# Kernel tuning notes

Hardware: AMD Instinct MI355X
Metric: run time of the kernel (lower is better)

## Reference

```python
import jax, jax.numpy as jnp
import numpy as np

B, S, H, U = 32, 2048, 1024, 1024


def setup_inputs() -> dict:
    key = jax.random.key(0)
    ks = jax.random.split(key, 8)
    sH = 1.0 / np.sqrt(H)
    sU = 1.0 / np.sqrt(U)
    return {
        "encoder_output": jax.random.normal(ks[0], (B, S, H), dtype=jnp.float32),
        "last_layer_h_n": jax.random.normal(ks[1], (B, H), dtype=jnp.float32),
        # torch Linear stores weight [out,in]; we store transposed [in,out] for x @ W
        "W1_w": jax.random.uniform(ks[2], (H, U), jnp.float32, -sH, sH),
        "W1_b": jax.random.uniform(ks[3], (U,), jnp.float32, -sH, sH),
        "W2_w": jax.random.uniform(ks[4], (H, U), jnp.float32, -sH, sH),
        "W2_b": jax.random.uniform(ks[5], (U,), jnp.float32, -sH, sH),
        "V_w": jax.random.uniform(ks[6], (U, 1), jnp.float32, -sU, sU),
        "V_b": jax.random.uniform(ks[7], (1,), jnp.float32, -sU, sU),
    }


def reference(encoder_output, last_layer_h_n, W1_w, W1_b, W2_w, W2_b, V_w, V_b):
    # proj_enc: [B,S,U]; proj_h: [B,1,U] (unsqueeze(1) broadcast)
    proj_enc = jnp.einsum("bsh,hu->bsu", encoder_output, W1_w) + W1_b
    proj_h = (last_layer_h_n @ W2_w + W2_b)[:, None, :]
    # score: [B,S,1]
    score = jnp.tanh(proj_enc + proj_h) @ V_w + V_b
    # softmax over the sequence axis (dim 1)
    attention_weights = jax.nn.softmax(score, axis=1)
    # NOTE: in the original module context_vector is always None (dead branch),
    # so the faithful output is attention_weights alone.
    return attention_weights
```

## Files before the change

kernel.cpp:

```cpp
#include <hip/hip_runtime.h>
#include <hip/hip_bf16.h>


typedef __bf16 bf16x8 __attribute__((ext_vector_type(8)));
typedef float  f32x4  __attribute__((ext_vector_type(4)));

#define HDIM 1024
#define UDIM 1024
#define SDIM 2048
#define MROWS 65536
#define BM 128
#define BN 128
#define BK 32
#define LDK 40

__device__ inline unsigned short f2bf(float x) {
    return __builtin_bit_cast(unsigned short, (__bf16)x);
}

__global__ void w1t_kernel(const float* __restrict__ W1, unsigned short* __restrict__ W1T) {
    __shared__ float tile[32][33];
    int bx = blockIdx.x;
    int by = blockIdx.y;
    int tx = threadIdx.x, ty = threadIdx.y;
#pragma unroll
    for (int r = 0; r < 4; ++r) {
        int h = by * 32 + ty + r * 8;
        int u = bx * 32 + tx;
        tile[ty + r * 8][tx] = W1[h * UDIM + u];
    }
    __syncthreads();
#pragma unroll
    for (int r = 0; r < 4; ++r) {
        int u = bx * 32 + ty + r * 8;
        int h = by * 32 + tx;
        W1T[u * HDIM + h] = f2bf(tile[tx][ty + r * 8]);
    }
}

__global__ void php_kernel(const float* __restrict__ hn, const float* __restrict__ W2,
                           float* __restrict__ php) {
    int u = (blockIdx.x & 3) * 256 + threadIdx.x;
    int b = blockIdx.y;
    int hc = blockIdx.z;
    int h0 = hc * 128;
    float acc = 0.f;
#pragma unroll 8
    for (int h = h0; h < h0 + 128; ++h)
        acc = fmaf(hn[b * HDIM + h], W2[h * UDIM + u], acc);
    php[(hc * 32 + b) * UDIM + u] = acc;
}

__global__ void ph_combine(const float* __restrict__ php, const float* __restrict__ W1b,
                           const float* __restrict__ W2b, float* __restrict__ ph) {
    int idx = blockIdx.x * 256 + threadIdx.x;
    int u = idx & (UDIM - 1);
    int b = idx >> 10;
    float acc = W1b[u] + W2b[u];
#pragma unroll
    for (int p = 0; p < 8; ++p) acc += php[(p * 32 + b) * UDIM + u];
    ph[idx] = acc;
}

__global__ __launch_bounds__(256) void score_kernel(
    const float* __restrict__ enc, const unsigned short* __restrict__ W1T,
    const float* __restrict__ ph, const float* __restrict__ Vw,
    float* __restrict__ part) {
    __shared__ unsigned short As[BM * LDK];
    __shared__ unsigned short Bs[BN * LDK];

    const int bx = blockIdx.x;
    const int tile_n = bx & 7;
    const int tile_m = bx >> 3;
    const int t = threadIdx.x;
    const int lane = t & 63;
    const int wid = t >> 6;
    const int wm = wid >> 1, wn = wid & 1;

    const int row0 = tile_m * BM;
    const int col0 = tile_n * BN;

    f32x4 acc[4][4];
#pragma unroll
    for (int i = 0; i < 4; ++i)
#pragma unroll
        for (int j = 0; j < 4; ++j)
            acc[i][j] = (f32x4){0.f, 0.f, 0.f, 0.f};

    const int mrow = lane & 15;
    const int kq = (lane >> 4) * 8;

    for (int kt = 0; kt < HDIM; kt += BK) {
        __syncthreads();
#pragma unroll
        for (int i = 0; i < 4; ++i) {
            int c = t + 256 * i;
            int r = c >> 3;
            int kc = (c & 7) * 4;
            const float4 f = *(const float4*)(enc + (size_t)(row0 + r) * HDIM + kt + kc);
            ushort4 h;
            h.x = f2bf(f.x); h.y = f2bf(f.y); h.z = f2bf(f.z); h.w = f2bf(f.w);
            *(ushort4*)(As + r * LDK + kc) = h;
        }
#pragma unroll
        for (int i = 0; i < 2; ++i) {
            int c = t + 256 * i;
            int r = c >> 2;
            int kc = (c & 3) * 8;
            const uint4 v = *(const uint4*)(W1T + (size_t)(col0 + r) * HDIM + kt + kc);
            *(uint4*)(Bs + r * LDK + kc) = v;
        }
        __syncthreads();

        bf16x8 a[4], bb[4];
#pragma unroll
        for (int i = 0; i < 4; ++i)
            a[i] = *reinterpret_cast<const bf16x8*>(As + (wm * 64 + i * 16 + mrow) * LDK + kq);
#pragma unroll
        for (int j = 0; j < 4; ++j)
            bb[j] = *reinterpret_cast<const bf16x8*>(Bs + (wn * 64 + j * 16 + mrow) * LDK + kq);
#pragma unroll
        for (int i = 0; i < 4; ++i)
#pragma unroll
            for (int j = 0; j < 4; ++j)
                acc[i][j] = __builtin_amdgcn_mfma_f32_16x16x32_bf16(a[i], bb[j], acc[i][j], 0, 0, 0);
    }

    const int b = row0 >> 11;
    const int colg = lane & 15;
    const int rowq = (lane >> 4) * 4;
    float vw[4], phv[4];
#pragma unroll
    for (int j = 0; j < 4; ++j) {
        int u = col0 + wn * 64 + j * 16 + colg;
        vw[j] = Vw[u];
        phv[j] = ph[b * UDIM + u];
    }
#pragma unroll
    for (int i = 0; i < 4; ++i) {
#pragma unroll
        for (int r = 0; r < 4; ++r) {
            float s = 0.f;
#pragma unroll
            for (int j = 0; j < 4; ++j) {
                float pe = acc[i][j][r] + phv[j];
                s += tanhf(pe) * vw[j];
            }
            s += __shfl_xor(s, 1);
            s += __shfl_xor(s, 2);
            s += __shfl_xor(s, 4);
            s += __shfl_xor(s, 8);
            if (colg == 0) {
                int row = row0 + wm * 64 + i * 16 + rowq + r;
                part[(size_t)(tile_n * 2 + wn) * MROWS + row] = s;
            }
        }
    }
}

__global__ void softmax_kernel(const float* __restrict__ part, float* __restrict__ out) {
    int b = blockIdx.x;
    int t = threadIdx.x;
    __shared__ float sred[4];
    float v[8];
    float lmax = -3.4e38f;
#pragma unroll
    for (int i = 0; i < 8; ++i) {
        int s = t + i * 256;
        float sum = 0.f;
#pragma unroll
        for (int p = 0; p < 16; ++p) sum += part[(size_t)p * MROWS + b * SDIM + s];
        v[i] = sum;
        lmax = fmaxf(lmax, sum);
    }
#pragma unroll
    for (int off = 1; off < 64; off <<= 1) lmax = fmaxf(lmax, __shfl_xor(lmax, off));
    if ((t & 63) == 0) sred[t >> 6] = lmax;
    __syncthreads();
    float bmax = fmaxf(fmaxf(sred[0], sred[1]), fmaxf(sred[2], sred[3]));
    __syncthreads();
    float lsum = 0.f;
#pragma unroll
    for (int i = 0; i < 8; ++i) {
        v[i] = expf(v[i] - bmax);
        lsum += v[i];
    }
#pragma unroll
    for (int off = 1; off < 64; off <<= 1) lsum += __shfl_xor(lsum, off);
    if ((t & 63) == 0) sred[t >> 6] = lsum;
    __syncthreads();
    float inv = 1.0f / (sred[0] + sred[1] + sred[2] + sred[3]);
#pragma unroll
    for (int i = 0; i < 8; ++i) out[b * SDIM + t + i * 256] = v[i] * inv;
}

extern "C" void kernel_launch(void* const* d_in, const int* in_sizes, int n_in,
                              void* d_out, int out_size, void* d_ws, size_t ws_size,
                              hipStream_t stream) {
    const float* enc = (const float*)d_in[0];
    const float* hn  = (const float*)d_in[1];
    const float* W1  = (const float*)d_in[2];
    const float* W1b = (const float*)d_in[3];
    const float* W2  = (const float*)d_in[4];
    const float* W2b = (const float*)d_in[5];
    const float* Vw  = (const float*)d_in[6];
    float* out = (float*)d_out;

    char* ws = (char*)d_ws;
    unsigned short* W1T = (unsigned short*)ws;
    float* ph   = (float*)(ws + (2u << 20));
    float* php  = (float*)(ws + (2u << 20) + (128u << 10));
    float* part = (float*)(ws + (2u << 20) + (128u << 10) + (1u << 20));

    w1t_kernel<<<dim3(32, 32), dim3(32, 8), 0, stream>>>(W1, W1T);
    php_kernel<<<dim3(4, 32, 8), 256, 0, stream>>>(hn, W2, php);
    ph_combine<<<128, 256, 0, stream>>>(php, W1b, W2b, ph);
    score_kernel<<<dim3(4096), 256, 0, stream>>>(enc, W1T, ph, Vw, part);
    softmax_kernel<<<32, 256, 0, stream>>>(part, out);
}
```

Measured before the change: 641.8 us.

## Pre-convert encoder to bf16 and load GEMM tiles via global_load_lds

Adds a separate pass that converts the fp32 encoder output to bf16 in workspace. The score GEMM then streams bf16 tiles straight into LDS with global_load_lds instead of loading fp32, converting in registers and writing LDS. Tile indices are also remapped so that neighbouring blocks share weight columns and encoder rows in L2. The price is an extra 384 MB of traffic (256 MB read, 128 MB written) plus 128 MB of workspace, and LDS loses its padding, which may cause bank conflicts; when workspace is too small the old fp32 path is used.

```diff
diff --git a/kernel.cpp b/kernel.cpp
--- a/kernel.cpp
+++ b/kernel.cpp
@@ -12,10 +12,26 @@
 #define BM 128
 #define BN 128
 #define BK 32
-#define LDK 40
 
 __device__ inline unsigned short f2bf(float x) {
     return __builtin_bit_cast(unsigned short, (__bf16)x);
+}
+
+#define GLDS16(gp, lp)                                                              \
+    __builtin_amdgcn_global_load_lds(                                               \
+        (const __attribute__((address_space(1))) unsigned int*)(gp),                \
+        (__attribute__((address_space(3))) unsigned int*)(lp), 16, 0, 0)
+
+__global__ __launch_bounds__(256) void cvt_kernel(const float* __restrict__ in,
+                                                  unsigned short* __restrict__ out) {
+    size_t i = ((size_t)blockIdx.x * 256 + threadIdx.x) * 8;
+    const float4 f0 = *(const float4*)(in + i);
+    const float4 f1 = *(const float4*)(in + i + 4);
+    ushort4 h0, h1;
+    h0.x = f2bf(f0.x); h0.y = f2bf(f0.y); h0.z = f2bf(f0.z); h0.w = f2bf(f0.w);
+    h1.x = f2bf(f1.x); h1.y = f2bf(f1.y); h1.z = f2bf(f1.z); h1.w = f2bf(f1.w);
+    *(ushort4*)(out + i) = h0;
+    *(ushort4*)(out + i + 4) = h1;
 }
 
 __global__ void w1t_kernel(const float* __restrict__ W1, unsigned short* __restrict__ W1T) {
@@ -63,15 +79,18 @@
 }
 
 __global__ __launch_bounds__(256) void score_kernel(
-    const float* __restrict__ enc, const unsigned short* __restrict__ W1T,
+    const unsigned short* __restrict__ encb, const unsigned short* __restrict__ W1T,
     const float* __restrict__ ph, const float* __restrict__ Vw,
     float* __restrict__ part) {
-    __shared__ unsigned short As[BM * LDK];
-    __shared__ unsigned short Bs[BN * LDK];
+    __shared__ unsigned short As[BM * BK];
+    __shared__ unsigned short Bs[BN * BK];
 
     const int bx = blockIdx.x;
-    const int tile_n = bx & 7;
-    const int tile_m = bx >> 3;
+    const int x = bx & 7;
+    const int k = bx >> 3;
+    const int tile_n = k & 7;
+    const int tile_m = (x << 6) | (k >> 3);
+
     const int t = threadIdx.x;
     const int lane = t & 63;
     const int wid = t >> 6;
@@ -90,40 +109,37 @@
     const int mrow = lane & 15;
     const int kq = (lane >> 4) * 8;
 
+    const int c0 = wid * 64 + lane;
+    const int c1 = c0 + 256;
+    const unsigned ldsA0 = (unsigned)(wid * 64) * 16;
+    const unsigned ldsA1 = ldsA0 + 256 * 16;
+
     for (int kt = 0; kt < HDIM; kt += BK) {
+        {
+            const unsigned short* ga0 = encb + (size_t)(row0 + (c0 >> 2)) * HDIM + kt + (c0 & 3) * 8;
+            const unsigned short* ga1 = encb + (size_t)(row0 + (c1 >> 2)) * HDIM + kt + (c1 & 3) * 8;
+            const unsigned short* gb0 = W1T + (size_t)(col0 + (c0 >> 2)) * HDIM + kt + (c0 & 3) * 8;
+            const unsigned short* gb1 = W1T + (size_t)(col0 + (c1 >> 2)) * HDIM + kt + (c1 & 3) * 8;
+            GLDS16(ga0, (char*)As + ldsA0);
+            GLDS16(ga1, (char*)As + ldsA1);
+            GLDS16(gb0, (char*)Bs + ldsA0);
+            GLDS16(gb1, (char*)Bs + ldsA1);
+        }
         __syncthreads();
-#pragma unroll
-        for (int i = 0; i < 4; ++i) {
-            int c = t + 256 * i;
-            int r = c >> 3;
-            int kc = (c & 7) * 4;
-            const float4 f = *(const float4*)(enc + (size_t)(row0 + r) * HDIM + kt + kc);
-            ushort4 h;
-            h.x = f2bf(f.x); h.y = f2bf(f.y); h.z = f2bf(f.z); h.w = f2bf(f.w);
-            *(ushort4*)(As + r * LDK + kc) = h;
-        }
-#pragma unroll
-        for (int i = 0; i < 2; ++i) {
-            int c = t + 256 * i;
-            int r = c >> 2;
-            int kc = (c & 3) * 8;
-            const uint4 v = *(const uint4*)(W1T + (size_t)(col0 + r) * HDIM + kt + kc);
-            *(uint4*)(Bs + r * LDK + kc) = v;
-        }
-        __syncthreads();
 
         bf16x8 a[4], bb[4];
 #pragma unroll
         for (int i = 0; i < 4; ++i)
-            a[i] = *reinterpret_cast<const bf16x8*>(As + (wm * 64 + i * 16 + mrow) * LDK + kq);
+            a[i] = *reinterpret_cast<const bf16x8*>(As + (wm * 64 + i * 16 + mrow) * BK + kq);
 #pragma unroll
         for (int j = 0; j < 4; ++j)
-            bb[j] = *reinterpret_cast<const bf16x8*>(Bs + (wn * 64 + j * 16 + mrow) * LDK + kq);
+            bb[j] = *reinterpret_cast<const bf16x8*>(Bs + (wn * 64 + j * 16 + mrow) * BK + kq);
 #pragma unroll
         for (int i = 0; i < 4; ++i)
 #pragma unroll
             for (int j = 0; j < 4; ++j)
                 acc[i][j] = __builtin_amdgcn_mfma_f32_16x16x32_bf16(a[i], bb[j], acc[i][j], 0, 0, 0);
+        __syncthreads();
     }
 
     const int b = row0 >> 11;
@@ -158,6 +174,103 @@
     }
 }
 
+#define LDK 40
+__global__ __launch_bounds__(256) void score_kernel_f32(
+    const float* __restrict__ enc, const unsigned short* __restrict__ W1T,
+    const float* __restrict__ ph, const float* __restrict__ Vw,
+    float* __restrict__ part) {
+    __shared__ unsigned short As[BM * LDK];
+    __shared__ unsigned short Bs[BN * LDK];
+
+    const int bx = blockIdx.x;
+    const int tile_n = bx & 7;
+    const int tile_m = bx >> 3;
+    const int t = threadIdx.x;
+    const int lane = t & 63;
+    const int wid = t >> 6;
+    const int wm = wid >> 1, wn = wid & 1;
+
+    const int row0 = tile_m * BM;
+    const int col0 = tile_n * BN;
+
+    f32x4 acc[4][4];
+#pragma unroll
+    for (int i = 0; i < 4; ++i)
+#pragma unroll
+        for (int j = 0; j < 4; ++j)
+            acc[i][j] = (f32x4){0.f, 0.f, 0.f, 0.f};
+
+    const int mrow = lane & 15;
+    const int kq = (lane >> 4) * 8;
+
+    for (int kt = 0; kt < HDIM; kt += BK) {
+        __syncthreads();
+#pragma unroll
+        for (int i = 0; i < 4; ++i) {
+            int c = t + 256 * i;
+            int r = c >> 3;
+            int kc = (c & 7) * 4;
+            const float4 f = *(const float4*)(enc + (size_t)(row0 + r) * HDIM + kt + kc);
+            ushort4 h;
+            h.x = f2bf(f.x); h.y = f2bf(f.y); h.z = f2bf(f.z); h.w = f2bf(f.w);
+            *(ushort4*)(As + r * LDK + kc) = h;
+        }
+#pragma unroll
+        for (int i = 0; i < 2; ++i) {
+            int c = t + 256 * i;
+            int r = c >> 2;
+            int kc = (c & 3) * 8;
+            const uint4 v = *(const uint4*)(W1T + (size_t)(col0 + r) * HDIM + kt + kc);
+            *(uint4*)(Bs + r * LDK + kc) = v;
+        }
+        __syncthreads();
+
+        bf16x8 a[4], bb[4];
+#pragma unroll
+        for (int i = 0; i < 4; ++i)
+            a[i] = *reinterpret_cast<const bf16x8*>(As + (wm * 64 + i * 16 + mrow) * LDK + kq);
+#pragma unroll
+        for (int j = 0; j < 4; ++j)
+            bb[j] = *reinterpret_cast<const bf16x8*>(Bs + (wn * 64 + j * 16 + mrow) * LDK + kq);
+#pragma unroll
+        for (int i = 0; i < 4; ++i)
+#pragma unroll
+            for (int j = 0; j < 4; ++j)
+                acc[i][j] = __builtin_amdgcn_mfma_f32_16x16x32_bf16(a[i], bb[j], acc[i][j], 0, 0, 0);
+    }
+
+    const int b = row0 >> 11;
+    const int colg = lane & 15;
+    const int rowq = (lane >> 4) * 4;
+    float vw[4], phv[4];
+#pragma unroll
+    for (int j = 0; j < 4; ++j) {
+        int u = col0 + wn * 64 + j * 16 + colg;
+        vw[j] = Vw[u];
+        phv[j] = ph[b * UDIM + u];
+    }
+#pragma unroll
+    for (int i = 0; i < 4; ++i) {
+#pragma unroll
+        for (int r = 0; r < 4; ++r) {
+            float s = 0.f;
+#pragma unroll
+            for (int j = 0; j < 4; ++j) {
+                float pe = acc[i][j][r] + phv[j];
+                s += tanhf(pe) * vw[j];
+            }
+            s += __shfl_xor(s, 1);
+            s += __shfl_xor(s, 2);
+            s += __shfl_xor(s, 4);
+            s += __shfl_xor(s, 8);
+            if (colg == 0) {
+                int row = row0 + wm * 64 + i * 16 + rowq + r;
+                part[(size_t)(tile_n * 2 + wn) * MROWS + row] = s;
+            }
+        }
+    }
+}
+
 __global__ void softmax_kernel(const float* __restrict__ part, float* __restrict__ out) {
     int b = blockIdx.x;
     int t = threadIdx.x;
@@ -207,14 +320,32 @@
     float* out = (float*)d_out;
 
     char* ws = (char*)d_ws;
-    unsigned short* W1T = (unsigned short*)ws;
-    float* ph   = (float*)(ws + (2u << 20));
-    float* php  = (float*)(ws + (2u << 20) + (128u << 10));
-    float* part = (float*)(ws + (2u << 20) + (128u << 10) + (1u << 20));
-
-    w1t_kernel<<<dim3(32, 32), dim3(32, 8), 0, stream>>>(W1, W1T);
-    php_kernel<<<dim3(4, 32, 8), 256, 0, stream>>>(hn, W2, php);
-    ph_combine<<<128, 256, 0, stream>>>(php, W1b, W2b, ph);
-    score_kernel<<<dim3(4096), 256, 0, stream>>>(enc, W1T, ph, Vw, part);
-    softmax_kernel<<<32, 256, 0, stream>>>(part, out);
-}
+    const size_t ENCB_BYTES = (size_t)MROWS * HDIM * 2;
+    const size_t NEED = ENCB_BYTES + (2u << 20) + (128u << 10) + (1u << 20) + (4u << 20);
+
+    if (ws_size >= NEED) {
+        unsigned short* encb = (unsigned short*)ws;
+        unsigned short* W1T  = (unsigned short*)(ws + ENCB_BYTES);
+        float* ph   = (float*)(ws + ENCB_BYTES + (2u << 20));
+        float* php  = (float*)(ws + ENCB_BYTES + (2u << 20) + (128u << 10));
+        float* part = (float*)(ws + ENCB_BYTES + (2u << 20) + (128u << 10) + (1u << 20));
+
+        cvt_kernel<<<32768, 256, 0, stream>>>(enc, encb);
+        w1t_kernel<<<dim3(32, 32), dim3(32, 8), 0, stream>>>(W1, W1T);
+        php_kernel<<<dim3(4, 32, 8), 256, 0, stream>>>(hn, W2, php);
+        ph_combine<<<128, 256, 0, stream>>>(php, W1b, W2b, ph);
+        score_kernel<<<dim3(4096), 256, 0, stream>>>(encb, W1T, ph, Vw, part);
+        softmax_kernel<<<32, 256, 0, stream>>>(part, out);
+    } else {
+        unsigned short* W1T = (unsigned short*)ws;
+        float* ph   = (float*)(ws + (2u << 20));
+        float* php  = (float*)(ws + (2u << 20) + (128u << 10));
+        float* part = (float*)(ws + (2u << 20) + (128u << 10) + (1u << 20));
+
+        w1t_kernel<<<dim3(32, 32), dim3(32, 8), 0, stream>>>(W1, W1T);
+        php_kernel<<<dim3(4, 32, 8), 256, 0, stream>>>(hn, W2, php);
+        ph_combine<<<128, 256, 0, stream>>>(php, W1b, W2b, ph);
+        score_kernel_f32<<<dim3(4096), 256, 0, stream>>>(enc, W1T, ph, Vw, part);
+        softmax_kernel<<<32, 256, 0, stream>>>(part, out);
+    }
+}
```

After: 615.0 us. 4.2% less time.
